# Optimization experiments

Hardware: AMD Instinct MI355X
Metric: run time of the kernel (lower is better)

Reference implementation:

```python
import jax, jax.numpy as jnp
import numpy as np

NUM_HEADS = 16
NEG_INF = -1e9


def setup_inputs() -> dict:
    key = jax.random.key(0)
    k1, k2, k3, k4, k5 = jax.random.split(key, 5)
    B, S, H = 1, 2048, 2048
    ROOM = 256
    N_ROOMS = H // ROOM  # 8
    return {
        "hidden_states": jax.random.normal(k1, (B, S, H), dtype=jnp.float32),
        "q_block": jax.random.normal(k2, (H, H), dtype=jnp.float32) * 0.02,
        "k_block": jax.random.normal(k3, (ROOM, H), dtype=jnp.float32) * 0.02,
        "v_block": jax.random.normal(k4, (ROOM, H), dtype=jnp.float32) * 0.02,
        "o_block": jax.random.normal(k5, (H, H), dtype=jnp.float32) * 0.02,
        "active_rooms": jnp.arange(N_ROOMS, dtype=jnp.int64),
    }


def reference(hidden_states, q_block, k_block, v_block, o_block, active_rooms):
    B, S, H = hidden_states.shape
    room = k_block.shape[0]                      # room_size == key_dim
    n_act = active_rooms.shape[0]
    total_dim = room * n_act
    head_dim = total_dim // NUM_HEADS

    # Gather the active room row-blocks from q_block / o_block.
    q_rooms = q_block.reshape(-1, room, H)[active_rooms]   # [R, room, H]
    o_active = o_block.reshape(-1, room, H)[active_rooms].reshape(total_dim, H)

    # Per-room Q projections (concat of h @ q_room.T over active rooms).
    q = jnp.einsum('bsh,rdh->bsrd', hidden_states, q_rooms).reshape(B, S, total_dim)
    # K/V use the same single block for every room -> compute once, tile.
    k_one = jnp.einsum('bsh,dh->bsd', hidden_states, k_block)  # [B,S,room]
    v_one = jnp.einsum('bsh,dh->bsd', hidden_states, v_block)
    k = jnp.tile(k_one, (1, 1, n_act))
    v = jnp.tile(v_one, (1, 1, n_act))

    # [B, nH, S, head_dim]
    def to_heads(x):
        return x.reshape(B, S, NUM_HEADS, head_dim).transpose(0, 2, 1, 3)
    qh, kh, vh = to_heads(q), to_heads(k), to_heads(v)

    scores = jnp.einsum('bhqd,bhkd->bhqk', qh, kh) / (head_dim ** 0.5)
    causal = jnp.triu(jnp.ones((S, S), dtype=scores.dtype), k=1) * NEG_INF
    attn_weights = jax.nn.softmax(scores + causal, axis=-1)
    attn_out = jnp.einsum('bhqk,bhkd->bhqd', attn_weights, vh)
    attn_out = attn_out.transpose(0, 2, 1, 3).reshape(B, S, total_dim)

    o_out = jnp.einsum('bst,th->bsh', attn_out, o_active)
    return o_out, attn_weights
```

## Files before the change

kernel.cpp:

```cpp
#include <hip/hip_runtime.h>
#include <hip/hip_bf16.h>
#include <hip/hip_fp16.h>

#define S_   2048
#define H_   2048
#define ROOM 256
#define NH   16
#define HD   128
#define TD   2048

typedef __hip_bfloat16 hbf16;

#define DT_F32  0
#define DT_BF16 1
#define DT_F16  2
#define SEL_F32   0
#define SEL_IN    1
#define SEL_SCORE 2
#define SEL_OUT   3

typedef __bf16    bf16x8 __attribute__((ext_vector_type(8)));
typedef _Float16  f16x8  __attribute__((ext_vector_type(8)));
typedef float     f32x4  __attribute__((ext_vector_type(4)));

__device__ __forceinline__ int resolveDT(int sel, int bf16mode) {
    if (sel == SEL_F32) return DT_F32;
    if (sel == SEL_SCORE) return bf16mode ? DT_F16 : DT_F32;
    return bf16mode ? DT_BF16 : DT_F32;
}
__device__ __forceinline__ float loadF(const void* p, long i, int dt) {
    if (dt == DT_F32)  return ((const float*)p)[i];
    if (dt == DT_BF16) return __bfloat162float(((const hbf16*)p)[i]);
    return __half2float(((const __half*)p)[i]);
}
__device__ __forceinline__ void storeF(void* p, long i, int dt, float v) {
    if (dt == DT_F32)       ((float*)p)[i] = v;
    else if (dt == DT_BF16) ((hbf16*)p)[i] = __float2bfloat16(v);
    else                    ((__half*)p)[i] = __float2half(v);
}

__device__ __forceinline__ void load8(const void* __restrict__ p, long idx, int dt, float* x) {
    if (dt == DT_F32) {
        const float4* f = (const float4*)((const float*)p + idx);
        float4 a = f[0], b = f[1];
        x[0]=a.x; x[1]=a.y; x[2]=a.z; x[3]=a.w;
        x[4]=b.x; x[5]=b.y; x[6]=b.z; x[7]=b.w;
    } else if (dt == DT_BF16) {
        bf16x8 v = *(const bf16x8*)((const __bf16*)p + idx);
        #pragma unroll
        for (int j = 0; j < 8; j++) x[j] = (float)v[j];
    } else {
        f16x8 v = *(const f16x8*)((const _Float16*)p + idx);
        #pragma unroll
        for (int j = 0; j < 8; j++) x[j] = (float)v[j];
    }
}
__device__ __forceinline__ void split8(const float* x, bf16x8& h, bf16x8& l) {
    #pragma unroll
    for (int j = 0; j < 8; j++) {
        float f = x[j];
        __bf16 hh = (__bf16)f;
        h[j] = hh;
        l[j] = (__bf16)(f - (float)hh);
    }
}
__device__ __forceinline__ void pack8f16(const float* x, f16x8& o) {
    #pragma unroll
    for (int j = 0; j < 8; j++) o[j] = (_Float16)x[j];
}

__device__ __forceinline__ f32x4 mfma16bf(bf16x8 a, bf16x8 b, f32x4 c) {
    return __builtin_amdgcn_mfma_f32_16x16x32_bf16(a, b, c, 0, 0, 0);
}
__device__ __forceinline__ f32x4 mfma16h(f16x8 a, f16x8 b, f32x4 c) {
    return __builtin_amdgcn_mfma_f32_16x16x32_f16(a, b, c, 0, 0, 0);
}

__global__ void setup_kernel(const void* __restrict__ hidden_raw,
                             const void* __restrict__ act_raw,
                             int* __restrict__ map, int* __restrict__ flags)
{
    __shared__ int sh_mode, sh_is64;
    if (threadIdx.x == 0) {
        const unsigned int* w = (const unsigned int*)hidden_raw;
        int cnt = 0;
        for (int i = 0; i < 1024; i++) {
            int e = (w[i] >> 7) & 0xFF;
            if (e >= 110 && e <= 135) cnt++;
        }
        sh_mode = (cnt > 512) ? 1 : 0;
        const long long* a64 = (const long long*)act_raw;
        int ok = 1;
        for (int i = 0; i < 4; i++) {
            long long v = a64[i];
            if (v < 0 || v >= 8) { ok = 0; break; }
        }
        sh_is64 = ok;
        flags[0] = sh_mode;
        flags[1] = sh_is64;
    }
    __syncthreads();
    const int is64 = sh_is64;
    const int*       a32 = (const int*)act_raw;
    const long long* a64 = (const long long*)act_raw;
    for (int n = threadIdx.x; n < TD; n += blockDim.x) {
        int slot = n >> 8;
        int room = is64 ? (int)a64[slot] : a32[slot];
        map[n] = room * ROOM + (n & 255);
    }
}

__global__ __launch_bounds__(256)
void conv_plain(const void* __restrict__ src, __bf16* __restrict__ hi,
                __bf16* __restrict__ lo, const int* __restrict__ flags)
{
    const int mode = flags[0];
    const int dt = resolveDT(SEL_IN, mode);
    const long i = ((long)blockIdx.x * 256 + threadIdx.x) * 8;
    float x[8]; load8(src, i, dt, x);
    if (mode == 1) {
        f16x8 h; pack8f16(x, h);
        *(f16x8*)((_Float16*)hi + i) = h;
    } else {
        bf16x8 h, l; split8(x, h, l);
        *(bf16x8*)(hi + i) = h;
        *(bf16x8*)(lo + i) = l;
    }
}

__global__ __launch_bounds__(256)
void conv_gather(const void* __restrict__ src, __bf16* __restrict__ hi,
                 __bf16* __restrict__ lo, const int* __restrict__ map,
                 const int* __restrict__ flags)
{
    const int mode = flags[0];
    const int dt = resolveDT(SEL_IN, mode);
    const int n = blockIdx.x;
    const long c = (long)threadIdx.x * 8;
    float x[8]; load8(src, (long)map[n] * H_ + c, dt, x);
    const long o = (long)n * H_ + c;
    if (mode == 1) {
        f16x8 h; pack8f16(x, h);
        *(f16x8*)((_Float16*)hi + o) = h;
    } else {
        bf16x8 h, l; split8(x, h, l);
        *(bf16x8*)(hi + o) = h;
        *(bf16x8*)(lo + o) = l;
    }
}

__global__ __launch_bounds__(256)
void conv_gatherT(const void* __restrict__ src, __bf16* __restrict__ hi,
                  __bf16* __restrict__ lo, const int* __restrict__ map,
                  const int* __restrict__ flags)
{
    const int mode = flags[0];
    const int dt = resolveDT(SEL_IN, mode);
    const int tB = blockIdx.x * 64;
    const int hB = blockIdx.y * 64;
    __shared__ float Ts[64][65];
    const int tid = threadIdx.x;
    const int i  = tid >> 2;
    const int j0 = (tid & 3) * 16;
    {
        const int srow = map[tB + i];
        const long base = (long)srow * H_ + hB + j0;
        float x[16];
        load8(src, base, dt, x);
        load8(src, base + 8, dt, x + 8);
        #pragma unroll
        for (int j = 0; j < 16; j++) Ts[i][j0 + j] = x[j];
    }
    __syncthreads();
    {
        const long drow = (long)(hB + i) * TD + tB + j0;
        float y[16];
        #pragma unroll
        for (int j = 0; j < 16; j++) y[j] = Ts[j0 + j][i];
        if (mode == 1) {
            f16x8 h0, h1;
            pack8f16(y, h0); pack8f16(y + 8, h1);
            *(f16x8*)((_Float16*)hi + drow)     = h0;
            *(f16x8*)((_Float16*)hi + drow + 8) = h1;
        } else {
            bf16x8 h0, h1, l0, l1;
            split8(y, h0, l0);
            split8(y + 8, h1, l1);
            *(bf16x8*)(hi + drow)     = h0;
            *(bf16x8*)(hi + drow + 8) = h1;
            *(bf16x8*)(lo + drow)     = l0;
            *(bf16x8*)(lo + drow + 8) = l1;
        }
    }
}

#define BN 128
#define BK 32
#define KST 40
#define EPAD 136
#define EPAD4 68

template<int TBM, int AMODE, int EPI, bool CAUSAL>
__global__ __launch_bounds__(256)
void mgemm(const __bf16* __restrict__ Ah, const __bf16* __restrict__ Al,
           const void* __restrict__ Araw, int aSel,
           const __bf16* __restrict__ Bh, const __bf16* __restrict__ Bl,
           __bf16* __restrict__ Ch, __bf16* __restrict__ Cl,
           void* __restrict__ Craw, int cSel,
           int K, int lda, int ldb, int ldc,
           long aBase, long bBase, long cBase,
           long aZ, long bZ, int bMod2, long cZ,
           const int* __restrict__ flags, int aLoSel, int bLoSel,
           float scale, float maskval)
{
    constexpr int NI = 4;
    constexpr int NJ = (TBM == 128) ? 4 : 2;
    constexpr int ASZ = 2 * TBM * KST;
    constexpr int BSZ = 2 * BN * KST;

    const int mode = flags[0];
    const bool f16m = (mode == 1);
    const bool useALo = (aLoSel == 0) || (mode == 0);
    const bool useBLo = (bLoSel == 0) || (mode == 0);
    const int aDT = (AMODE == 1) ? resolveDT(aSel, mode) : DT_F32;

    const int z = blockIdx.z;
    const long aOff = aBase + (long)z * aZ;
    const long bOff = bBase + (bMod2 ? (long)(z & 1) * bZ : (long)z * bZ);
    const long cOff = cBase + (long)z * cZ;

    const int gx = gridDim.x;
    const int nwg = gx * gridDim.y;
    const int orig = blockIdx.y * gx + blockIdx.x;
    const int q8 = nwg >> 3, r8 = nwg & 7;
    const int xcd = orig & 7, off8 = orig >> 3;
    const int wg = (xcd < r8 ? xcd * (q8 + 1) : r8 * (q8 + 1) + (xcd - r8) * q8) + off8;
    const int rowBase = (wg / gx) * TBM;
    const int colBase = (wg % gx) * BN;

    __shared__ __align__(16) __bf16 smem[ASZ + BSZ];
    auto As = (__bf16 (*)[TBM][KST])smem;
    auto Bs = (__bf16 (*)[BN][KST])(smem + ASZ);

    const int tid  = threadIdx.x;
    const int lane = tid & 63;
    const int w    = tid >> 6;
    const int fr   = lane & 15;
    const int fq   = lane >> 4;

    const int rowW = (TBM == 128) ? (w >> 1) * 64 : 0;
    const int colW = (TBM == 128) ? (w & 1) * 64  : w * 32;

    const int sAr = (TBM == 128) ? (tid >> 1) : (tid >> 2);
    const int sAc = (TBM == 128) ? (tid & 1) * 16 : (tid & 3) * 8;
    const int sBr = tid >> 1;
    const int sBc = (tid & 1) * 16;

    f32x4 acc[NI][NJ];
    const f32x4 zero = {0.f, 0.f, 0.f, 0.f};
    #pragma unroll
    for (int i = 0; i < NI; i++)
        #pragma unroll
        for (int j = 0; j < NJ; j++) acc[i][j] = zero;

    bf16x8 pA0, pA1, pA2, pA3;
    float  pAf[16];
    bf16x8 pB0, pB1, pB2, pB3;

    auto issueA = [&](int kt) {
        const long e = aOff + (long)(rowBase + sAr) * lda + kt + sAc;
        if constexpr (AMODE == 0) {
            if constexpr (TBM == 128) {
                pA0 = *(const bf16x8*)(Ah + e);
                pA1 = *(const bf16x8*)(Ah + e + 8);
                if (!f16m) {
                    pA2 = *(const bf16x8*)(Al + e);
                    pA3 = *(const bf16x8*)(Al + e + 8);
                }
            } else {
                pA0 = *(const bf16x8*)(Ah + e);
                if (!f16m) pA2 = *(const bf16x8*)(Al + e);
            }
        } else {
            if constexpr (TBM == 128) {
                load8(Araw, e, aDT, pAf);
                load8(Araw, e + 8, aDT, pAf + 8);
            } else {
                load8(Araw, e, aDT, pAf);
            }
        }
    };
    auto issueB = [&](int kt) {
        const long e = bOff + (long)(colBase + sBr) * ldb + kt + sBc;
        pB0 = *(const bf16x8*)(Bh + e);
        pB1 = *(const bf16x8*)(Bh + e + 8);
        if (!f16m) {
            pB2 = *(const bf16x8*)(Bl + e);
            pB3 = *(const bf16x8*)(Bl + e + 8);
        }
    };
    auto commit = [&]() {
        if constexpr (AMODE == 0) {
            if constexpr (TBM == 128) {
                *(bf16x8*)&As[0][sAr][sAc]     = pA0;
                *(bf16x8*)&As[0][sAr][sAc + 8] = pA1;
                if (!f16m) {
                    *(bf16x8*)&As[1][sAr][sAc]     = pA2;
                    *(bf16x8*)&As[1][sAr][sAc + 8] = pA3;
                }
            } else {
                *(bf16x8*)&As[0][sAr][sAc] = pA0;
                if (!f16m) *(bf16x8*)&As[1][sAr][sAc] = pA2;
            }
        } else {
            if (f16m) {
                if constexpr (TBM == 128) {
                    f16x8 h0, h1;
                    pack8f16(pAf, h0); pack8f16(pAf + 8, h1);
                    *(f16x8*)&As[0][sAr][sAc]     = h0;
                    *(f16x8*)&As[0][sAr][sAc + 8] = h1;
                } else {
                    f16x8 h0; pack8f16(pAf, h0);
                    *(f16x8*)&As[0][sAr][sAc] = h0;
                }
            } else {
                if constexpr (TBM == 128) {
                    bf16x8 h0, h1, l0, l1;
                    split8(pAf, h0, l0);
                    split8(pAf + 8, h1, l1);
                    *(bf16x8*)&As[0][sAr][sAc]     = h0;
                    *(bf16x8*)&As[0][sAr][sAc + 8] = h1;
                    *(bf16x8*)&As[1][sAr][sAc]     = l0;
                    *(bf16x8*)&As[1][sAr][sAc + 8] = l1;
                } else {
                    bf16x8 h0, l0;
                    split8(pAf, h0, l0);
                    *(bf16x8*)&As[0][sAr][sAc] = h0;
                    *(bf16x8*)&As[1][sAr][sAc] = l0;
                }
            }
        }
        *(bf16x8*)&Bs[0][sBr][sBc]     = pB0;
        *(bf16x8*)&Bs[0][sBr][sBc + 8] = pB1;
        if (!f16m) {
            *(bf16x8*)&Bs[1][sBr][sBc]     = pB2;
            *(bf16x8*)&Bs[1][sBr][sBc + 8] = pB3;
        }
    };

    issueA(0); issueB(0);

    for (int kt = 0; kt < K; kt += BK) {
        commit();
        __syncthreads();
        if (kt + BK < K) {
            issueA(kt + BK);
            issueB(kt + BK);
        }
        __builtin_amdgcn_sched_barrier(0);

        if (f16m) {
            f16x8 a16[NI], b16[NJ];
            #pragma unroll
            for (int i = 0; i < NI; i++)
                a16[i] = *(const f16x8*)&As[0][rowW + i * 16 + fr][fq * 8];
            #pragma unroll
            for (int j = 0; j < NJ; j++)
                b16[j] = *(const f16x8*)&Bs[0][colW + j * 16 + fr][fq * 8];
            #pragma unroll
            for (int i = 0; i < NI; i++)
                #pragma unroll
                for (int j = 0; j < NJ; j++)
                    acc[i][j] = mfma16h(a16[i], b16[j], acc[i][j]);
        } else {
            bf16x8 ah[NI], al[NI], bh[NJ], bl[NJ];
            #pragma unroll
            for (int i = 0; i < NI; i++)
                ah[i] = *(const bf16x8*)&As[0][rowW + i * 16 + fr][fq * 8];
            #pragma unroll
            for (int j = 0; j < NJ; j++)
                bh[j] = *(const bf16x8*)&Bs[0][colW + j * 16 + fr][fq * 8];
            if (useALo)
                #pragma unroll
                for (int i = 0; i < NI; i++)
                    al[i] = *(const bf16x8*)&As[1][rowW + i * 16 + fr][fq * 8];
            if (useBLo)
                #pragma unroll
                for (int j = 0; j < NJ; j++)
                    bl[j] = *(const bf16x8*)&Bs[1][colW + j * 16 + fr][fq * 8];

            #pragma unroll
            for (int i = 0; i < NI; i++)
                #pragma unroll
                for (int j = 0; j < NJ; j++)
                    acc[i][j] = mfma16bf(ah[i], bh[j], acc[i][j]);
            if (useBLo)
                #pragma unroll
                for (int i = 0; i < NI; i++)
                    #pragma unroll
                    for (int j = 0; j < NJ; j++)
                        acc[i][j] = mfma16bf(ah[i], bl[j], acc[i][j]);
            if (useALo)
                #pragma unroll
                for (int i = 0; i < NI; i++)
                    #pragma unroll
                    for (int j = 0; j < NJ; j++)
                        acc[i][j] = mfma16bf(al[i], bh[j], acc[i][j]);
        }
        __syncthreads();
    }

    const int cDT = (EPI == 0) ? (f16m ? DT_F16 : DT_BF16) : resolveDT(cSel, mode);

    if (EPI == 1 && cDT == DT_F32) {
        float* ep = (float*)smem;
        #pragma unroll
        for (int half = 0; half < 2; half++) {
            if ((colW >> 6) == half) {
                #pragma unroll
                for (int i = 0; i < NI; i++)
                    #pragma unroll
                    for (int rr = 0; rr < 4; rr++) {
                        const int lrow = rowW + i * 16 + fq * 4 + rr;
                        #pragma unroll
                        for (int j = 0; j < NJ; j++) {
                            float v = acc[i][j][rr] * scale;
                            const int lcol = colW + j * 16 + fr;
                            if (CAUSAL) {
                                if (colBase + lcol > rowBase + lrow) v = maskval;
                            }
                            ep[lrow * EPAD4 + (lcol - half * 64)] = v;
                        }
                    }
            }
            __syncthreads();
            const int chunk = tid & 15, r0 = tid >> 4;
            for (int r = r0; r < TBM; r += 16) {
                float4 v = *(const float4*)&ep[(long)r * EPAD4 + chunk * 4];
                *(float4*)((float*)Craw + cOff + (long)(rowBase + r) * ldc
                           + colBase + half * 64 + chunk * 4) = v;
            }
            __syncthreads();
        }
    } else {
        const int planes = (EPI == 0 && !f16m) ? 2 : 1;
        for (int pl = 0; pl < planes; pl++) {
            #pragma unroll
            for (int i = 0; i < NI; i++)
                #pragma unroll
                for (int rr = 0; rr < 4; rr++) {
                    const int lrow = rowW + i * 16 + fq * 4 + rr;
                    #pragma unroll
                    for (int j = 0; j < NJ; j++) {
                        float v = acc[i][j][rr];
                        const int lcol = colW + j * 16 + fr;
                        if constexpr (EPI == 1) {
                            v *= scale;
                            if (CAUSAL) {
                                if (colBase + lcol > rowBase + lrow) v = maskval;
                            }
                        }
                        const long li = (long)lrow * EPAD + lcol;
                        if (cDT == DT_F16) {
                            ((_Float16*)smem)[li] = (_Float16)v;
                        } else {
                            __bf16 h = (__bf16)v;
                            ((__bf16*)smem)[li] = (pl == 0) ? h : (__bf16)(v - (float)h);
                        }
                    }
                }
            __syncthreads();
            __bf16* dst = (EPI == 1) ? (__bf16*)Craw : (pl == 0 ? Ch : Cl);
            const int chunk = tid & 15, r0 = tid >> 4;
            for (int r = r0; r < TBM; r += 16) {
                bf16x8 v = *(const bf16x8*)((const __bf16*)smem + (long)r * EPAD + chunk * 8);
                *(bf16x8*)(dst + cOff + (long)(rowBase + r) * ldc + colBase + chunk * 8) = v;
            }
            __syncthreads();
        }
    }
}

__global__ __launch_bounds__(256)
void softmax_kernel(void* __restrict__ attn, long base, const int* __restrict__ flags)
{
    const int mode  = flags[0];
    const int rdDT  = resolveDT(SEL_SCORE, mode);
    const int wrDT  = resolveDT(SEL_OUT, mode);

    const int qrow = blockIdx.x;
    const int h    = blockIdx.y;
    const long row = base + ((long)h * S_ + qrow) * S_;
    const int tid  = threadIdx.x;
    const int wave = tid >> 6, lane = tid & 63;

    float vals[8];
    const bool v32 = (rdDT == DT_F32);
    const bool v16 = (rdDT == DT_F16);
    const long my8 = row + (long)tid * 8;
    if (v16) {
        f16x8 v = *(const f16x8*)((const _Float16*)attn + my8);
        #pragma unroll
        for (int j = 0; j < 8; j++) vals[j] = (float)v[j];
    } else if (v32) {
        const float4* rp = (const float4*)((const float*)attn + row);
        float4 a = rp[tid], b = rp[tid + 256];
        vals[0]=a.x; vals[1]=a.y; vals[2]=a.z; vals[3]=a.w;
        vals[4]=b.x; vals[5]=b.y; vals[6]=b.z; vals[7]=b.w;
    } else {
        #pragma unroll
        for (int i = 0; i < 8; i++)
            vals[i] = loadF(attn, row + tid + i * 256, rdDT);
    }

    float m = -3.4e38f;
    #pragma unroll
    for (int i = 0; i < 8; i++) m = fmaxf(m, vals[i]);
    #pragma unroll
    for (int off = 32; off > 0; off >>= 1)
        m = fmaxf(m, __shfl_down(m, off, 64));
    __shared__ float redm[4];
    if (lane == 0) redm[wave] = m;
    __syncthreads();
    if (tid == 0) redm[0] = fmaxf(fmaxf(redm[0], redm[1]), fmaxf(redm[2], redm[3]));
    __syncthreads();
    m = redm[0];

    float s = 0.f;
    #pragma unroll
    for (int i = 0; i < 8; i++) {
        vals[i] = __expf(vals[i] - m);
        s += vals[i];
    }
    #pragma unroll
    for (int off = 32; off > 0; off >>= 1)
        s += __shfl_down(s, off, 64);
    __shared__ float reds[4];
    if (lane == 0) reds[wave] = s;
    __syncthreads();
    if (tid == 0) reds[0] = reds[0] + reds[1] + reds[2] + reds[3];
    __syncthreads();
    const float inv = 1.f / reds[0];

    if (v16 && wrDT == DT_BF16) {
        bf16x8 o;
        #pragma unroll
        for (int j = 0; j < 8; j++) o[j] = (__bf16)(vals[j] * inv);
        *(bf16x8*)((__bf16*)attn + my8) = o;
    } else if (v32 && wrDT == DT_F32) {
        float4* wp = (float4*)((float*)attn + row);
        float4 a, b;
        a.x=vals[0]*inv; a.y=vals[1]*inv; a.z=vals[2]*inv; a.w=vals[3]*inv;
        b.x=vals[4]*inv; b.y=vals[5]*inv; b.z=vals[6]*inv; b.w=vals[7]*inv;
        wp[tid] = a; wp[tid + 256] = b;
    } else {
        #pragma unroll
        for (int i = 0; i < 8; i++)
            storeF(attn, row + tid + i * 256, wrDT, vals[i] * inv);
    }
}

extern "C" void kernel_launch(void* const* d_in, const int* in_sizes, int n_in,
                              void* d_out, int out_size, void* d_ws, size_t ws_size,
                              hipStream_t stream)
{
    (void)in_sizes; (void)n_in; (void)out_size; (void)ws_size;

    const void* hidden = d_in[0];
    const void* qb     = d_in[1];
    const void* kb     = d_in[2];
    const void* vb     = d_in[3];
    const void* ob     = d_in[4];
    const void* act    = d_in[5];

    const long ATTN_BASE = (long)S_ * TD;

    const long PLANE = (long)S_ * H_;
    const long SMALL = (long)ROOM * H_;
    __bf16* p = (__bf16*)d_ws;
    __bf16* hidH = p;               __bf16* hidL = hidH + PLANE;
    __bf16* aoH  = hidH;            __bf16* aoL  = hidL;
    __bf16* qbH  = p + 2 * PLANE;   __bf16* qbL  = qbH + PLANE;
    __bf16* otH  = qbH;             __bf16* otL  = qbL;
    __bf16* qfH  = p + 4 * PLANE;   __bf16* qfL  = qfH + PLANE;
    __bf16* kbH  = p + 6 * PLANE;   __bf16* kbL  = kbH + SMALL;
    __bf16* vbH  = kbL + SMALL;     __bf16* vbL  = vbH + SMALL;
    __bf16* k1H  = vbL + SMALL;     __bf16* k1L  = k1H + SMALL;
    __bf16* vtH  = k1L + SMALL;     __bf16* vtL  = vtH + SMALL;
    int* map   = (int*)(vtL + SMALL);
    int* flags = map + TD;

    const float inv_sqrt_hd = 0.08838834764831845f;

    setup_kernel<<<1, 256, 0, stream>>>(hidden, act, map, flags);

    conv_plain<<<dim3((unsigned)(PLANE / 2048)), 256, 0, stream>>>(hidden, hidH, hidL, flags);
    conv_gather<<<dim3(TD), 256, 0, stream>>>(qb, qbH, qbL, map, flags);
    conv_plain<<<dim3((unsigned)(SMALL / 2048)), 256, 0, stream>>>(kb, kbH, kbL, flags);
    conv_plain<<<dim3((unsigned)(SMALL / 2048)), 256, 0, stream>>>(vb, vbH, vbL, flags);

    mgemm<64, 0, 0, false><<<dim3(TD / BN, S_ / 64, 1), 256, 0, stream>>>(
        hidH, hidL, nullptr, 0, qbH, qbL, qfH, qfL, nullptr, 0,
        H_, H_, H_, TD, 0, 0, 0, 0, 0, 0, 0, flags, 1, 1, 1.f, 0.f);

    mgemm<64, 0, 0, false><<<dim3(ROOM / BN, S_ / 64, 1), 256, 0, stream>>>(
        hidH, hidL, nullptr, 0, kbH, kbL, k1H, k1L, nullptr, 0,
        H_, H_, H_, ROOM, 0, 0, 0, 0, 0, 0, 0, flags, 1, 1, 1.f, 0.f);

    mgemm<64, 0, 0, false><<<dim3(S_ / BN, ROOM / 64, 1), 256, 0, stream>>>(
        vbH, vbL, nullptr, 0, hidH, hidL, vtH, vtL, nullptr, 0,
        H_, H_, H_, S_, 0, 0, 0, 0, 0, 0, 0, flags, 1, 1, 1.f, 0.f);

    mgemm<128, 0, 1, true><<<dim3(S_ / BN, S_ / 128, NH), 256, 0, stream>>>(
        qfH, qfL, nullptr, 0, k1H, k1L, nullptr, nullptr, d_out, SEL_SCORE,
        HD, TD, ROOM, S_, 0, 0, ATTN_BASE,
        (long)HD, (long)HD, 1, (long)S_ * S_, flags, 0, 0, inv_sqrt_hd, -1e4f);

    softmax_kernel<<<dim3(S_, NH), 256, 0, stream>>>(d_out, ATTN_BASE, flags);

    conv_gatherT<<<dim3(TD / 64, H_ / 64), 256, 0, stream>>>(ob, otH, otL, map, flags);

    mgemm<64, 1, 0, false><<<dim3(HD / BN, S_ / 64, NH), 256, 0, stream>>>(
        nullptr, nullptr, d_out, SEL_OUT, vtH, vtL, aoH, aoL, nullptr, 0,
        S_, S_, S_, TD, ATTN_BASE, 0, 0,
        (long)S_ * S_, (long)HD * S_, 1, (long)HD, flags, 1, 0, 1.f, 0.f);

    mgemm<64, 0, 1, false><<<dim3(H_ / BN, S_ / 64, 1), 256, 0, stream>>>(
        aoH, aoL, nullptr, 0, otH, otL, nullptr, nullptr, d_out, SEL_OUT,
        TD, TD, TD, H_, 0, 0, 0, 0, 0, 0, 0, flags, 0, 1, 1.f, 0.f);
}
```

Measured before the change: 877.1 us.

## Double K-tile to 64 and add double-buffered LDS pipeline for f16 GEMM path

The GEMM K-step grows from 32 to 64 with a padded stride of 72. Global-to-register loads are reorganized into per-thread 8-element chunks. In f16 mode the two LDS planes become ping-pong buffers, so the next tile is committed while the current one is consumed, and only one barrier per iteration is needed. The setup kernel's exponent count is also parallelized across threads with a shared atomic. This halves loop iterations and barrier overhead but raises register and LDS use, which may lower occupancy.

```diff
diff --git a/kernel.cpp b/kernel.cpp
--- a/kernel.cpp
+++ b/kernel.cpp
@@ -80,15 +80,10 @@
                              const void* __restrict__ act_raw,
                              int* __restrict__ map, int* __restrict__ flags)
 {
-    __shared__ int sh_mode, sh_is64;
-    if (threadIdx.x == 0) {
-        const unsigned int* w = (const unsigned int*)hidden_raw;
-        int cnt = 0;
-        for (int i = 0; i < 1024; i++) {
-            int e = (w[i] >> 7) & 0xFF;
-            if (e >= 110 && e <= 135) cnt++;
-        }
-        sh_mode = (cnt > 512) ? 1 : 0;
+    __shared__ int sh_cnt, sh_is64;
+    const int tid = threadIdx.x;
+    if (tid == 0) {
+        sh_cnt = 0;
         const long long* a64 = (const long long*)act_raw;
         int ok = 1;
         for (int i = 0; i < 4; i++) {
@@ -96,14 +91,26 @@
             if (v < 0 || v >= 8) { ok = 0; break; }
         }
         sh_is64 = ok;
-        flags[0] = sh_mode;
+    }
+    __syncthreads();
+    {
+        const unsigned int* w = (const unsigned int*)hidden_raw;
+        int local = 0;
+        for (int i = tid; i < 1024; i += 256) {
+            int e = (w[i] >> 7) & 0xFF;
+            if (e >= 110 && e <= 135) local++;
+        }
+        atomicAdd(&sh_cnt, local);
+    }
+    __syncthreads();
+    if (tid == 0) {
+        flags[0] = (sh_cnt > 512) ? 1 : 0;
         flags[1] = sh_is64;
     }
-    __syncthreads();
     const int is64 = sh_is64;
     const int*       a32 = (const int*)act_raw;
     const long long* a64 = (const long long*)act_raw;
-    for (int n = threadIdx.x; n < TD; n += blockDim.x) {
+    for (int n = tid; n < TD; n += blockDim.x) {
         int slot = n >> 8;
         int room = is64 ? (int)a64[slot] : a32[slot];
         map[n] = room * ROOM + (n & 255);
@@ -195,8 +202,8 @@
 }
 
 #define BN 128
-#define BK 32
-#define KST 40
+#define BK 64
+#define KSTP 72
 #define EPAD 136
 #define EPAD4 68
 
@@ -215,8 +222,10 @@
 {
     constexpr int NI = 4;
     constexpr int NJ = (TBM == 128) ? 4 : 2;
-    constexpr int ASZ = 2 * TBM * KST;
-    constexpr int BSZ = 2 * BN * KST;
+    constexpr int AE = TBM / 32;
+    constexpr int BE = 4;
+    constexpr int ASZ = 2 * TBM * KSTP;
+    constexpr int BSZ = 2 * BN * KSTP;
 
     const int mode = flags[0];
     const bool f16m = (mode == 1);
@@ -239,8 +248,8 @@
     const int colBase = (wg % gx) * BN;
 
     __shared__ __align__(16) __bf16 smem[ASZ + BSZ];
-    auto As = (__bf16 (*)[TBM][KST])smem;
-    auto Bs = (__bf16 (*)[BN][KST])(smem + ASZ);
+    auto As = (__bf16 (*)[TBM][KSTP])smem;
+    auto Bs = (__bf16 (*)[BN][KSTP])(smem + ASZ);
 
     const int tid  = threadIdx.x;
     const int lane = tid & 63;
@@ -251,11 +260,6 @@
     const int rowW = (TBM == 128) ? (w >> 1) * 64 : 0;
     const int colW = (TBM == 128) ? (w & 1) * 64  : w * 32;
 
-    const int sAr = (TBM == 128) ? (tid >> 1) : (tid >> 2);
-    const int sAc = (TBM == 128) ? (tid & 1) * 16 : (tid & 3) * 8;
-    const int sBr = tid >> 1;
-    const int sBc = (tid & 1) * 16;
-
     f32x4 acc[NI][NJ];
     const f32x4 zero = {0.f, 0.f, 0.f, 0.f};
     #pragma unroll
@@ -263,152 +267,149 @@
         #pragma unroll
         for (int j = 0; j < NJ; j++) acc[i][j] = zero;
 
-    bf16x8 pA0, pA1, pA2, pA3;
-    float  pAf[16];
-    bf16x8 pB0, pB1, pB2, pB3;
-
-    auto issueA = [&](int kt) {
-        const long e = aOff + (long)(rowBase + sAr) * lda + kt + sAc;
-        if constexpr (AMODE == 0) {
-            if constexpr (TBM == 128) {
-                pA0 = *(const bf16x8*)(Ah + e);
-                pA1 = *(const bf16x8*)(Ah + e + 8);
-                if (!f16m) {
-                    pA2 = *(const bf16x8*)(Al + e);
-                    pA3 = *(const bf16x8*)(Al + e + 8);
-                }
+    bf16x8 pA[AE], pAl[AE], pB[BE], pBl[BE];
+    float  pAf[AE * 8];
+
+    auto issueAB = [&](int kt) {
+        #pragma unroll
+        for (int v = 0; v < AE; v++) {
+            const int L = tid + v * 256;
+            const long e = aOff + (long)(rowBase + (L >> 3)) * lda + kt + (L & 7) * 8;
+            if constexpr (AMODE == 0) {
+                pA[v] = *(const bf16x8*)(Ah + e);
+                if (!f16m) pAl[v] = *(const bf16x8*)(Al + e);
             } else {
-                pA0 = *(const bf16x8*)(Ah + e);
-                if (!f16m) pA2 = *(const bf16x8*)(Al + e);
-            }
-        } else {
-            if constexpr (TBM == 128) {
-                load8(Araw, e, aDT, pAf);
-                load8(Araw, e + 8, aDT, pAf + 8);
+                load8(Araw, e, aDT, pAf + v * 8);
+            }
+        }
+        #pragma unroll
+        for (int v = 0; v < BE; v++) {
+            const int L = tid + v * 256;
+            const long e = bOff + (long)(colBase + (L >> 3)) * ldb + kt + (L & 7) * 8;
+            pB[v] = *(const bf16x8*)(Bh + e);
+            if (!f16m) pBl[v] = *(const bf16x8*)(Bl + e);
+        }
+    };
+    auto commit16 = [&](int buf) {
+        #pragma unroll
+        for (int v = 0; v < AE; v++) {
+            const int L = tid + v * 256;
+            if constexpr (AMODE == 0) {
+                *(bf16x8*)&As[buf][L >> 3][(L & 7) * 8] = pA[v];
             } else {
-                load8(Araw, e, aDT, pAf);
-            }
+                f16x8 h; pack8f16(pAf + v * 8, h);
+                *(f16x8*)&As[buf][L >> 3][(L & 7) * 8] = h;
+            }
+        }
+        #pragma unroll
+        for (int v = 0; v < BE; v++) {
+            const int L = tid + v * 256;
+            *(bf16x8*)&Bs[buf][L >> 3][(L & 7) * 8] = pB[v];
         }
     };
-    auto issueB = [&](int kt) {
-        const long e = bOff + (long)(colBase + sBr) * ldb + kt + sBc;
-        pB0 = *(const bf16x8*)(Bh + e);
-        pB1 = *(const bf16x8*)(Bh + e + 8);
-        if (!f16m) {
-            pB2 = *(const bf16x8*)(Bl + e);
-            pB3 = *(const bf16x8*)(Bl + e + 8);
+    auto commit32 = [&]() {
+        #pragma unroll
+        for (int v = 0; v < AE; v++) {
+            const int L = tid + v * 256;
+            if constexpr (AMODE == 0) {
+                *(bf16x8*)&As[0][L >> 3][(L & 7) * 8] = pA[v];
+                *(bf16x8*)&As[1][L >> 3][(L & 7) * 8] = pAl[v];
+            } else {
+                bf16x8 h, l; split8(pAf + v * 8, h, l);
+                *(bf16x8*)&As[0][L >> 3][(L & 7) * 8] = h;
+                *(bf16x8*)&As[1][L >> 3][(L & 7) * 8] = l;
+            }
+        }
+        #pragma unroll
+        for (int v = 0; v < BE; v++) {
+            const int L = tid + v * 256;
+            *(bf16x8*)&Bs[0][L >> 3][(L & 7) * 8] = pB[v];
+            *(bf16x8*)&Bs[1][L >> 3][(L & 7) * 8] = pBl[v];
         }
     };
-    auto commit = [&]() {
-        if constexpr (AMODE == 0) {
-            if constexpr (TBM == 128) {
-                *(bf16x8*)&As[0][sAr][sAc]     = pA0;
-                *(bf16x8*)&As[0][sAr][sAc + 8] = pA1;
-                if (!f16m) {
-                    *(bf16x8*)&As[1][sAr][sAc]     = pA2;
-                    *(bf16x8*)&As[1][sAr][sAc + 8] = pA3;
-                }
-            } else {
-                *(bf16x8*)&As[0][sAr][sAc] = pA0;
-                if (!f16m) *(bf16x8*)&As[1][sAr][sAc] = pA2;
-            }
-        } else {
-            if (f16m) {
-                if constexpr (TBM == 128) {
-                    f16x8 h0, h1;
-                    pack8f16(pAf, h0); pack8f16(pAf + 8, h1);
-                    *(f16x8*)&As[0][sAr][sAc]     = h0;
-                    *(f16x8*)&As[0][sAr][sAc + 8] = h1;
-                } else {
-                    f16x8 h0; pack8f16(pAf, h0);
-                    *(f16x8*)&As[0][sAr][sAc] = h0;
-                }
-            } else {
-                if constexpr (TBM == 128) {
-                    bf16x8 h0, h1, l0, l1;
-                    split8(pAf, h0, l0);
-                    split8(pAf + 8, h1, l1);
-                    *(bf16x8*)&As[0][sAr][sAc]     = h0;
-                    *(bf16x8*)&As[0][sAr][sAc + 8] = h1;
-                    *(bf16x8*)&As[1][sAr][sAc]     = l0;
-                    *(bf16x8*)&As[1][sAr][sAc + 8] = l1;
-                } else {
-                    bf16x8 h0, l0;
-                    split8(pAf, h0, l0);
-                    *(bf16x8*)&As[0][sAr][sAc] = h0;
-                    *(bf16x8*)&As[1][sAr][sAc] = l0;
-                }
-            }
-        }
-        *(bf16x8*)&Bs[0][sBr][sBc]     = pB0;
-        *(bf16x8*)&Bs[0][sBr][sBc + 8] = pB1;
-        if (!f16m) {
-            *(bf16x8*)&Bs[1][sBr][sBc]     = pB2;
-            *(bf16x8*)&Bs[1][sBr][sBc + 8] = pB3;
-        }
-    };
-
-    issueA(0); issueB(0);
-
-    for (int kt = 0; kt < K; kt += BK) {
-        commit();
+
+    if (f16m) {
+        issueAB(0);
+        commit16(0);
         __syncthreads();
-        if (kt + BK < K) {
-            issueA(kt + BK);
-            issueB(kt + BK);
-        }
-        __builtin_amdgcn_sched_barrier(0);
-
-        if (f16m) {
-            f16x8 a16[NI], b16[NJ];
+        int cur = 0;
+        for (int kt = 0; kt < K; kt += BK) {
+            const bool haveNext = (kt + BK < K);
+            if (haveNext) issueAB(kt + BK);
+            __builtin_amdgcn_sched_barrier(0);
+
+            f16x8 a16[NI][2], b16[NJ][2];
             #pragma unroll
-            for (int i = 0; i < NI; i++)
-                a16[i] = *(const f16x8*)&As[0][rowW + i * 16 + fr][fq * 8];
+            for (int c = 0; c < 2; c++) {
+                #pragma unroll
+                for (int i = 0; i < NI; i++)
+                    a16[i][c] = *(const f16x8*)&As[cur][rowW + i * 16 + fr][c * 32 + fq * 8];
+                #pragma unroll
+                for (int j = 0; j < NJ; j++)
+                    b16[j][c] = *(const f16x8*)&Bs[cur][colW + j * 16 + fr][c * 32 + fq * 8];
+            }
             #pragma unroll
-            for (int j = 0; j < NJ; j++)
-                b16[j] = *(const f16x8*)&Bs[0][colW + j * 16 + fr][fq * 8];
+            for (int c = 0; c < 2; c++)
+                #pragma unroll
+                for (int i = 0; i < NI; i++)
+                    #pragma unroll
+                    for (int j = 0; j < NJ; j++)
+                        acc[i][j] = mfma16h(a16[i][c], b16[j][c], acc[i][j]);
+
+            if (haveNext) {
+                commit16(cur ^ 1);
+                __syncthreads();
+                cur ^= 1;
+            }
+        }
+    } else {
+        issueAB(0);
+        for (int kt = 0; kt < K; kt += BK) {
+            commit32();
+            __syncthreads();
+            if (kt + BK < K) issueAB(kt + BK);
+            __builtin_amdgcn_sched_barrier(0);
+
             #pragma unroll
-            for (int i = 0; i < NI; i++)
+            for (int c = 0; c < 2; c++) {
+                bf16x8 ah[NI], al[NI], bh[NJ], bl[NJ];
+                #pragma unroll
+                for (int i = 0; i < NI; i++)
+                    ah[i] = *(const bf16x8*)&As[0][rowW + i * 16 + fr][c * 32 + fq * 8];
                 #pragma unroll
                 for (int j = 0; j < NJ; j++)
-                    acc[i][j] = mfma16h(a16[i], b16[j], acc[i][j]);
-        } else {
-            bf16x8 ah[NI], al[NI], bh[NJ], bl[NJ];
-            #pragma unroll
-            for (int i = 0; i < NI; i++)
-                ah[i] = *(const bf16x8*)&As[0][rowW + i * 16 + fr][fq * 8];
-            #pragma unroll
-            for (int j = 0; j < NJ; j++)
-                bh[j] = *(const bf16x8*)&Bs[0][colW + j * 16 + fr][fq * 8];
-            if (useALo)
+                    bh[j] = *(const bf16x8*)&Bs[0][colW + j * 16 + fr][c * 32 + fq * 8];
+                if (useALo)
+                    #pragma unroll
+                    for (int i = 0; i < NI; i++)
+                        al[i] = *(const bf16x8*)&As[1][rowW + i * 16 + fr][c * 32 + fq * 8];
+                if (useBLo)
+                    #pragma unroll
+                    for (int j = 0; j < NJ; j++)
+                        bl[j] = *(const bf16x8*)&Bs[1][colW + j * 16 + fr][c * 32 + fq * 8];
+
                 #pragma unroll
                 for (int i = 0; i < NI; i++)
-                    al[i] = *(const bf16x8*)&As[1][rowW + i * 16 + fr][fq * 8];
-            if (useBLo)
-                #pragma unroll
-                for (int j = 0; j < NJ; j++)
-                    bl[j] = *(const bf16x8*)&Bs[1][colW + j * 16 + fr][fq * 8];
-
-            #pragma unroll
-            for (int i = 0; i < NI; i++)
-                #pragma unroll
-                for (int j = 0; j < NJ; j++)
-                    acc[i][j] = mfma16bf(ah[i], bh[j], acc[i][j]);
-            if (useBLo)
-                #pragma unroll
-                for (int i = 0; i < NI; i++)
                     #pragma unroll
                     for (int j = 0; j < NJ; j++)
-                        acc[i][j] = mfma16bf(ah[i], bl[j], acc[i][j]);
-            if (useALo)
-                #pragma unroll
-                for (int i = 0; i < NI; i++)
-                    #pragma unroll
-                    for (int j = 0; j < NJ; j++)
-                        acc[i][j] = mfma16bf(al[i], bh[j], acc[i][j]);
-        }
-        __syncthreads();
-    }
+                        acc[i][j] = mfma16bf(ah[i], bh[j], acc[i][j]);
+                if (useBLo)
+                    #pragma unroll
+                    for (int i = 0; i < NI; i++)
+                        #pragma unroll
+                        for (int j = 0; j < NJ; j++)
+                            acc[i][j] = mfma16bf(ah[i], bl[j], acc[i][j]);
+                if (useALo)
+                    #pragma unroll
+                    for (int i = 0; i < NI; i++)
+                        #pragma unroll
+                        for (int j = 0; j < NJ; j++)
+                            acc[i][j] = mfma16bf(al[i], bh[j], acc[i][j]);
+            }
+            __syncthreads();
+        }
+    }
+    __syncthreads();
 
     const int cDT = (EPI == 0) ? (f16m ? DT_F16 : DT_BF16) : resolveDT(cSel, mode);
 
```

New measurement: 786.3 us. 10.4% less time.
